# Performance work log

Hardware: AMD Instinct MI355X
Metric: run time of the kernel (lower is better)

The kernel has to match this reference:

```python
import jax, jax.numpy as jnp
import numpy as np

N_FEATURES = 256
SEQ_LEN = 128
N_HIDDEN = 30
N_LAYERS = 2
BATCH = 1024


def _lstm_layer(x, w_ih, w_hh, b_ih, b_hh):
    # x: [B, T, I]; w_ih: [4H, I]; w_hh: [4H, H]; biases: [4H]
    # PyTorch gate order: i, f, g, o
    B = x.shape[0]
    H = w_hh.shape[1]
    # precompute input contribution for all timesteps: [B, T, 4H]
    xg = jnp.einsum('bti,gi->btg', x, w_ih) + (b_ih + b_hh)
    xg = jnp.swapaxes(xg, 0, 1)  # [T, B, 4H]

    def step(carry, xg_t):
        h, c = carry
        gates = xg_t + h @ w_hh.T  # [B, 4H]
        i, f, g, o = jnp.split(gates, 4, axis=-1)
        i = jax.nn.sigmoid(i)
        f = jax.nn.sigmoid(f)
        g = jnp.tanh(g)
        o = jax.nn.sigmoid(o)
        c = f * c + i * g
        h = o * jnp.tanh(c)
        return (h, c), h

    h0 = jnp.zeros((B, H), dtype=x.dtype)
    c0 = jnp.zeros((B, H), dtype=x.dtype)
    _, hs = jax.lax.scan(step, (h0, c0), xg)
    return jnp.swapaxes(hs, 0, 1)  # [B, T, H]


def setup_inputs() -> dict:
    key = jax.random.key(0)
    ks = jax.random.split(key, 12)
    s_in = 1.0 / np.sqrt(N_HIDDEN)
    G = 4 * N_HIDDEN
    inp = {
        'x': jax.random.normal(ks[0], (BATCH, SEQ_LEN, N_FEATURES), dtype=jnp.float32),
        'w_ih0': jax.random.uniform(ks[1], (G, N_FEATURES), jnp.float32, -s_in, s_in),
        'w_hh0': jax.random.uniform(ks[2], (G, N_HIDDEN), jnp.float32, -s_in, s_in),
        'b_ih0': jax.random.uniform(ks[3], (G,), jnp.float32, -s_in, s_in),
        'b_hh0': jax.random.uniform(ks[4], (G,), jnp.float32, -s_in, s_in),
        'w_ih1': jax.random.uniform(ks[5], (G, N_HIDDEN), jnp.float32, -s_in, s_in),
        'w_hh1': jax.random.uniform(ks[6], (G, N_HIDDEN), jnp.float32, -s_in, s_in),
        'b_ih1': jax.random.uniform(ks[7], (G,), jnp.float32, -s_in, s_in),
        'b_hh1': jax.random.uniform(ks[8], (G,), jnp.float32, -s_in, s_in),
        'w_lin': jax.random.uniform(ks[9], (1, N_HIDDEN * SEQ_LEN), jnp.float32, -s_in, s_in),
        'b_lin': jax.random.uniform(ks[10], (1,), jnp.float32, -s_in, s_in),
    }
    return inp


def reference(x, w_ih0, w_hh0, b_ih0, b_hh0, w_ih1, w_hh1, b_ih1, b_hh1, w_lin, b_lin):
    h1 = _lstm_layer(x, w_ih0, w_hh0, b_ih0, b_hh0)   # [B, T, H]
    h2 = _lstm_layer(h1, w_ih1, w_hh1, b_ih1, b_hh1)  # [B, T, H]
    flat = h2.reshape(h2.shape[0], -1)                 # [B, T*H]
    return flat @ w_lin.T + b_lin                      # [B, 1]
```

## Files before the change

### kernel.cpp

```cpp
#include <hip/hip_runtime.h>

#define T_SEQ 128
#define NF 256
#define NH 30
#define NG 120
#define NBATCH 1024
#define M_ROWS (NBATCH * T_SEQ)

#define BIAS_OFF 0
#define BHI_OFF  1024
#define BLO_OFF  (BHI_OFF + 65536)
#define XG_OFF_B (BLO_OFF + 65536)

typedef __attribute__((ext_vector_type(8))) short short8;
typedef __attribute__((ext_vector_type(4))) float float4v;

__device__ __forceinline__ short bf16_of(float f) {
  union { float f; unsigned u; } v; v.f = f;
  unsigned r = v.u + 0x7fffu + ((v.u >> 16) & 1u);
  return (short)(r >> 16);
}
__device__ __forceinline__ float f_of_bf16(short s) {
  union { unsigned u; float f; } v; v.u = ((unsigned)(unsigned short)s) << 16;
  return v.f;
}

__device__ __forceinline__ float rl(float v, int j) {
  return __int_as_float(__builtin_amdgcn_readlane(__float_as_int(v), j));
}
__device__ __forceinline__ float fast_rcp(float x) { return __builtin_amdgcn_rcpf(x); }
__device__ __forceinline__ float act_mix(float x, float kIn, float kOut, float cOut) {
  float e = __expf(-kIn * x);
  float r = fast_rcp(1.0f + e);
  return fmaf(kOut, r, cOut);
}
__device__ __forceinline__ float tanh_fast(float x) {
  float e = __expf(-2.0f * x);
  float r = fast_rcp(1.0f + e);
  return fmaf(2.0f, r, -1.0f);
}

__global__ void prep_kernel(const float* __restrict__ w_ih0,
                            const float* __restrict__ b_ih0,
                            const float* __restrict__ b_hh0,
                            unsigned char* __restrict__ ws) {
  int gid = blockIdx.x * 256 + threadIdx.x;
  float* bias = (float*)(ws + BIAS_OFF);
  if (gid < 128) bias[gid] = (gid < NG) ? (b_ih0[gid] + b_hh0[gid]) : 0.0f;

  int lane = gid & 63;
  int ts = gid >> 6;
  int t = ts >> 3, s = ts & 7;
  int n = s * 16 + (lane & 15);
  int k0 = t * 32 + (lane >> 4) * 8;

  short8 hi, lo;
#pragma unroll
  for (int j = 0; j < 8; ++j) {
    float v = (n < NG) ? w_ih0[n * NF + k0 + j] : 0.0f;
    short h = bf16_of(v);
    hi[j] = h;
    lo[j] = bf16_of(v - f_of_bf16(h));
  }
  *(short8*)(ws + BHI_OFF + (size_t)gid * 16) = hi;
  *(short8*)(ws + BLO_OFF + (size_t)gid * 16) = lo;
}

__global__ __launch_bounds__(256, 3) void gemm_xg(const float* __restrict__ x,
                                                  const unsigned char* __restrict__ ws,
                                                  float* __restrict__ xg) {
  __shared__ short lds_B[2][8 * 2 * 64 * 8];
  const int tid = threadIdx.x;
  const int lane = tid & 63;
  const int wave = tid >> 6;
  const int r15 = lane & 15;
  const int quad = lane >> 4;
  const int rowbase = blockIdx.x * 128 + wave * 32;

  const short* __restrict__ Bhi = (const short*)(ws + BHI_OFF);
  const short* __restrict__ Blo = (const short*)(ws + BLO_OFF);
  const float* __restrict__ bias = (const float*)(ws + BIAS_OFF);

  float4v acc[2][8];
#pragma unroll
  for (int s = 0; s < 8; ++s) {
    float b = bias[s * 16 + r15];
    float4v bv = {b, b, b, b};
    acc[0][s] = bv;
    acc[1][s] = bv;
  }

  const float* xptr[2];
  xptr[0] = x + (size_t)(rowbase + r15) * NF + quad * 8;
  xptr[1] = x + (size_t)(rowbase + 16 + r15) * NF + quad * 8;

#pragma unroll
  for (int i = 0; i < 2; ++i) {
    int s = wave * 2 + i;
    const short* ghi = Bhi + ((size_t)(0 * 8 + s) * 64 + lane) * 8;
    const short* glo = Blo + ((size_t)(0 * 8 + s) * 64 + lane) * 8;
    short* lhi = &lds_B[0][(s * 2 + 0) * 64 * 8];
    short* llo = &lds_B[0][(s * 2 + 1) * 64 * 8];
    __builtin_amdgcn_global_load_lds((const __attribute__((address_space(1))) void*)ghi,
                                     (__attribute__((address_space(3))) void*)lhi, 16, 0, 0);
    __builtin_amdgcn_global_load_lds((const __attribute__((address_space(1))) void*)glo,
                                     (__attribute__((address_space(3))) void*)llo, 16, 0, 0);
  }

  short8 ahi[2], alo[2];
#pragma unroll
  for (int g = 0; g < 2; ++g) {
    float4 p0 = *(const float4*)(xptr[g] + 0);
    float4 p1 = *(const float4*)(xptr[g] + 4);
    float f[8] = {p0.x, p0.y, p0.z, p0.w, p1.x, p1.y, p1.z, p1.w};
#pragma unroll
    for (int j = 0; j < 8; ++j) {
      short h = bf16_of(f[j]);
      ahi[g][j] = h;
      alo[g][j] = bf16_of(f[j] - f_of_bf16(h));
    }
  }
  __syncthreads();

  for (int t = 0; t < 8; ++t) {
    const int buf = t & 1;
    float4 anx[2][2];
    if (t < 7) {
#pragma unroll
      for (int i = 0; i < 2; ++i) {
        int s = wave * 2 + i;
        const short* ghi = Bhi + ((size_t)((t + 1) * 8 + s) * 64 + lane) * 8;
        const short* glo = Blo + ((size_t)((t + 1) * 8 + s) * 64 + lane) * 8;
        short* lhi = &lds_B[buf ^ 1][(s * 2 + 0) * 64 * 8];
        short* llo = &lds_B[buf ^ 1][(s * 2 + 1) * 64 * 8];
        __builtin_amdgcn_global_load_lds((const __attribute__((address_space(1))) void*)ghi,
                                         (__attribute__((address_space(3))) void*)lhi, 16, 0, 0);
        __builtin_amdgcn_global_load_lds((const __attribute__((address_space(1))) void*)glo,
                                         (__attribute__((address_space(3))) void*)llo, 16, 0, 0);
      }
#pragma unroll
      for (int g = 0; g < 2; ++g) {
        anx[g][0] = *(const float4*)(xptr[g] + (t + 1) * 32);
        anx[g][1] = *(const float4*)(xptr[g] + (t + 1) * 32 + 4);
      }
    }

#pragma unroll
    for (int s = 0; s < 8; ++s) {
      const short8 bh = *(const short8*)&lds_B[buf][((s * 2 + 0) * 64 + lane) * 8];
      const short8 bl = *(const short8*)&lds_B[buf][((s * 2 + 1) * 64 + lane) * 8];
#pragma unroll
      for (int g = 0; g < 2; ++g) {
        acc[g][s] = __builtin_amdgcn_mfma_f32_16x16x32_bf16(ahi[g], bh, acc[g][s], 0, 0, 0);
        acc[g][s] = __builtin_amdgcn_mfma_f32_16x16x32_bf16(ahi[g], bl, acc[g][s], 0, 0, 0);
        acc[g][s] = __builtin_amdgcn_mfma_f32_16x16x32_bf16(alo[g], bh, acc[g][s], 0, 0, 0);
      }
    }

    if (t < 7) {
#pragma unroll
      for (int g = 0; g < 2; ++g) {
        float f[8] = {anx[g][0].x, anx[g][0].y, anx[g][0].z, anx[g][0].w,
                      anx[g][1].x, anx[g][1].y, anx[g][1].z, anx[g][1].w};
#pragma unroll
        for (int j = 0; j < 8; ++j) {
          short h = bf16_of(f[j]);
          ahi[g][j] = h;
          alo[g][j] = bf16_of(f[j] - f_of_bf16(h));
        }
      }
    }
    __syncthreads();
  }

#pragma unroll
  for (int g = 0; g < 2; ++g) {
    const int row0 = rowbase + g * 16 + quad * 4;
#pragma unroll
    for (int s = 0; s < 8; ++s) {
      const int col = s * 16 + r15;
      if (col < NG) {
#pragma unroll
        for (int i = 0; i < 4; ++i) {
          xg[(size_t)(row0 + i) * NG + col] = acc[g][s][i];
        }
      }
    }
  }
}

__global__ __launch_bounds__(64) void lstm_fused(const float* __restrict__ xg,
                                                 const float* __restrict__ w_hh0,
                                                 const float* __restrict__ w_ih1,
                                                 const float* __restrict__ w_hh1,
                                                 const float* __restrict__ b_ih1,
                                                 const float* __restrict__ b_hh1,
                                                 const float* __restrict__ w_lin,
                                                 const float* __restrict__ b_lin,
                                                 float* __restrict__ out) {
  const int b = blockIdx.x;
  const int lane = threadIdx.x;
  const bool hiHalf = lane >= 32;
  const int l = hiHalf ? (lane - 32) : lane;
  const int lc = (l < NH) ? l : (NH - 1);
  const int gA = hiHalf ? (60 + lc) : lc;
  const int gB = gA + NH;

  const float kInA = hiHalf ? 2.0f : 1.0f;
  const float kOutA = hiHalf ? 2.0f : 1.0f;
  const float cOutA = hiHalf ? -1.0f : 0.0f;

  float wA0[NH], wB0[NH], vA1[NH], vB1[NH], uA1[NH], uB1[NH];
#pragma unroll
  for (int j = 0; j < NH; ++j) {
    wA0[j] = w_hh0[gA * NH + j];
    wB0[j] = w_hh0[gB * NH + j];
    vA1[j] = w_ih1[gA * NH + j];
    vB1[j] = w_ih1[gB * NH + j];
    uA1[j] = w_hh1[gA * NH + j];
    uB1[j] = w_hh1[gB * NH + j];
  }
  const float bA1 = b_ih1[gA] + b_hh1[gA];
  const float bB1 = b_ih1[gB] + b_hh1[gB];

  float h0 = 0.0f, c0 = 0.0f, h1 = 0.0f, c1 = 0.0f, acc = 0.0f;
  const float* __restrict__ xgb = xg + (size_t)b * T_SEQ * NG;

  float xa[4], xb[4], wlr[4];
#pragma unroll
  for (int p = 0; p < 3; ++p) {
    xa[p] = xgb[p * NG + gA];
    xb[p] = xgb[p * NG + gB];
    wlr[p] = w_lin[p * NH + lc];
  }

#pragma unroll 4
  for (int t = 0; t < T_SEQ; ++t) {
    const int cur = t & 3;
    const int nxt = (t + 3) & 3;
    const int tp = (t + 3 < T_SEQ) ? (t + 3) : (T_SEQ - 1);
    float pxa = xgb[tp * NG + gA];
    float pxb = xgb[tp * NG + gB];
    float pwl = w_lin[tp * NH + lc];

    float sA = xa[cur], sB = xb[cur], sA2 = 0.0f, sB2 = 0.0f;
#pragma unroll
    for (int j = 0; j < NH; j += 2) {
      float hj = rl(h0, j);
      float hj1 = rl(h0, j + 1);
      sA = fmaf(hj, wA0[j], sA);
      sB = fmaf(hj, wB0[j], sB);
      sA2 = fmaf(hj1, wA0[j + 1], sA2);
      sB2 = fmaf(hj1, wB0[j + 1], sB2);
    }
    sA += sA2;
    sB += sB2;
    float aA = act_mix(sA, kInA, kOutA, cOutA);
    float aB = act_mix(sB, 1.0f, 1.0f, 0.0f);
    float gg = __shfl_down(aA, 32);
    float oo = __shfl_down(aB, 32);
    c0 = fmaf(aB, c0, aA * gg);
    h0 = oo * tanh_fast(c0);

    float sv = bA1, sv2 = 0.0f, svB = bB1, svB2 = 0.0f;
    float su = 0.0f, su2 = 0.0f, suB = 0.0f, suB2 = 0.0f;
#pragma unroll
    for (int j = 0; j < NH; j += 2) {
      float xj = rl(h0, j);
      float xj1 = rl(h0, j + 1);
      float hj = rl(h1, j);
      float hj1 = rl(h1, j + 1);
      sv = fmaf(xj, vA1[j], sv);
      svB = fmaf(xj, vB1[j], svB);
      sv2 = fmaf(xj1, vA1[j + 1], sv2);
      svB2 = fmaf(xj1, vB1[j + 1], svB2);
      su = fmaf(hj, uA1[j], su);
      suB = fmaf(hj, uB1[j], suB);
      su2 = fmaf(hj1, uA1[j + 1], su2);
      suB2 = fmaf(hj1, uB1[j + 1], suB2);
    }
    float s1A = (sv + sv2) + (su + su2);
    float s1B = (svB + svB2) + (suB + suB2);
    float a1A = act_mix(s1A, kInA, kOutA, cOutA);
    float a1B = act_mix(s1B, 1.0f, 1.0f, 0.0f);
    float gg1 = __shfl_down(a1A, 32);
    float oo1 = __shfl_down(a1B, 32);
    c1 = fmaf(a1B, c1, a1A * gg1);
    h1 = oo1 * tanh_fast(c1);

    acc = fmaf(h1, wlr[cur], acc);

    xa[nxt] = pxa;
    xb[nxt] = pxb;
    wlr[nxt] = pwl;
  }

  if (lane >= NH) acc = 0.0f;
#pragma unroll
  for (int off = 32; off > 0; off >>= 1) acc += __shfl_xor(acc, off);
  if (lane == 0) out[b] = acc + b_lin[0];
}

extern "C" void kernel_launch(void* const* d_in, const int* in_sizes, int n_in,
                              void* d_out, int out_size, void* d_ws, size_t ws_size,
                              hipStream_t stream) {
  (void)in_sizes; (void)n_in; (void)out_size; (void)ws_size;
  const float* x     = (const float*)d_in[0];
  const float* w_ih0 = (const float*)d_in[1];
  const float* w_hh0 = (const float*)d_in[2];
  const float* b_ih0 = (const float*)d_in[3];
  const float* b_hh0 = (const float*)d_in[4];
  const float* w_ih1 = (const float*)d_in[5];
  const float* w_hh1 = (const float*)d_in[6];
  const float* b_ih1 = (const float*)d_in[7];
  const float* b_hh1 = (const float*)d_in[8];
  const float* w_lin = (const float*)d_in[9];
  const float* b_lin = (const float*)d_in[10];
  unsigned char* ws = (unsigned char*)d_ws;
  float* out = (float*)d_out;
  float* xg = (float*)(ws + XG_OFF_B);

  prep_kernel<<<16, 256, 0, stream>>>(w_ih0, b_ih0, b_hh0, ws);
  gemm_xg<<<M_ROWS / 128, 256, 0, stream>>>(x, ws, xg);
  lstm_fused<<<NBATCH, 64, 0, stream>>>(xg, w_hh0, w_ih1, w_hh1,
                                        b_ih1, b_hh1, w_lin, b_lin, out);
}
```

Baseline: 294.1 us.

## Broadcast hidden state via LDS and use packed FP32 FMA in LSTM recurrence

Replaces per-element readlane broadcasts of the hidden state with a write to shared memory followed by vector reads. The recurrent dot products now use packed two-wide FMAs. Input-projection gate columns are interleaved in the prep kernel so each lane fetches its two gate preactivations with one 8-byte load, and activations use exp2 directly. The aim is to cut instruction count on the serial per-timestep chain, at the cost of LDS round-trip latency inside the dependency chain.

```diff
diff --git a/kernel.cpp b/kernel.cpp
--- a/kernel.cpp
+++ b/kernel.cpp
@@ -13,6 +13,7 @@
 #define XG_OFF_B (BLO_OFF + 65536)
 
 typedef __attribute__((ext_vector_type(8))) short short8;
+typedef __attribute__((ext_vector_type(2))) float float2v;
 typedef __attribute__((ext_vector_type(4))) float float4v;
 
 __device__ __forceinline__ short bf16_of(float f) {
@@ -25,19 +26,24 @@
   return v.f;
 }
 
-__device__ __forceinline__ float rl(float v, int j) {
-  return __int_as_float(__builtin_amdgcn_readlane(__float_as_int(v), j));
-}
 __device__ __forceinline__ float fast_rcp(float x) { return __builtin_amdgcn_rcpf(x); }
-__device__ __forceinline__ float act_mix(float x, float kIn, float kOut, float cOut) {
-  float e = __expf(-kIn * x);
-  float r = fast_rcp(1.0f + e);
-  return fmaf(kOut, r, cOut);
+
+#define L2E 1.4426950408889634f
+__device__ __forceinline__ float sigm_fast(float x) {
+  float e = __builtin_amdgcn_exp2f(-L2E * x);
+  return fast_rcp(1.0f + e);
+}
+__device__ __forceinline__ float act_a(float x, float kIn_l2, float kOut, float cOut) {
+  float e = __builtin_amdgcn_exp2f(-kIn_l2 * x);
+  return fmaf(kOut, fast_rcp(1.0f + e), cOut);
 }
 __device__ __forceinline__ float tanh_fast(float x) {
-  float e = __expf(-2.0f * x);
-  float r = fast_rcp(1.0f + e);
-  return fmaf(2.0f, r, -1.0f);
+  float e = __builtin_amdgcn_exp2f(-2.0f * L2E * x);
+  return fmaf(2.0f, fast_rcp(1.0f + e), -1.0f);
+}
+
+__device__ __forceinline__ float2v fma2(float2v a, float2v b, float2v c) {
+  return __builtin_elementwise_fma(a, b, c);
 }
 
 __global__ void prep_kernel(const float* __restrict__ w_ih0,
@@ -46,18 +52,22 @@
                             unsigned char* __restrict__ ws) {
   int gid = blockIdx.x * 256 + threadIdx.x;
   float* bias = (float*)(ws + BIAS_OFF);
-  if (gid < 128) bias[gid] = (gid < NG) ? (b_ih0[gid] + b_hh0[gid]) : 0.0f;
+  if (gid < 128) {
+    int og = (gid & 3) * NH + (gid >> 2);
+    bias[gid] = (gid < NG) ? (b_ih0[og] + b_hh0[og]) : 0.0f;
+  }
 
   int lane = gid & 63;
   int ts = gid >> 6;
   int t = ts >> 3, s = ts & 7;
   int n = s * 16 + (lane & 15);
+  int orig = (n & 3) * NH + (n >> 2);
   int k0 = t * 32 + (lane >> 4) * 8;
 
   short8 hi, lo;
 #pragma unroll
   for (int j = 0; j < 8; ++j) {
-    float v = (n < NG) ? w_ih0[n * NF + k0 + j] : 0.0f;
+    float v = (n < NG) ? w_ih0[orig * NF + k0 + j] : 0.0f;
     short h = bf16_of(v);
     hi[j] = h;
     lo[j] = bf16_of(v - f_of_bf16(h));
@@ -189,15 +199,17 @@
   }
 }
 
-__global__ __launch_bounds__(64) void lstm_fused(const float* __restrict__ xg,
-                                                 const float* __restrict__ w_hh0,
-                                                 const float* __restrict__ w_ih1,
-                                                 const float* __restrict__ w_hh1,
-                                                 const float* __restrict__ b_ih1,
-                                                 const float* __restrict__ b_hh1,
-                                                 const float* __restrict__ w_lin,
-                                                 const float* __restrict__ b_lin,
-                                                 float* __restrict__ out) {
+__global__ __launch_bounds__(64, 1) void lstm_fused(const float* __restrict__ xg,
+                                                    const float* __restrict__ w_hh0,
+                                                    const float* __restrict__ w_ih1,
+                                                    const float* __restrict__ w_hh1,
+                                                    const float* __restrict__ b_ih1,
+                                                    const float* __restrict__ b_hh1,
+                                                    const float* __restrict__ w_lin,
+                                                    const float* __restrict__ b_lin,
+                                                    float* __restrict__ out) {
+  __shared__ __align__(16) float hbuf0[32];
+  __shared__ __align__(16) float hbuf1[32];
   const int b = blockIdx.x;
   const int lane = threadIdx.x;
   const bool hiHalf = lane >= 32;
@@ -206,31 +218,39 @@
   const int gA = hiHalf ? (60 + lc) : lc;
   const int gB = gA + NH;
 
-  const float kInA = hiHalf ? 2.0f : 1.0f;
+  const float kInA = (hiHalf ? 2.0f : 1.0f) * L2E;
   const float kOutA = hiHalf ? 2.0f : 1.0f;
   const float cOutA = hiHalf ? -1.0f : 0.0f;
 
-  float wA0[NH], wB0[NH], vA1[NH], vB1[NH], uA1[NH], uB1[NH];
-#pragma unroll
-  for (int j = 0; j < NH; ++j) {
-    wA0[j] = w_hh0[gA * NH + j];
-    wB0[j] = w_hh0[gB * NH + j];
-    vA1[j] = w_ih1[gA * NH + j];
-    vB1[j] = w_ih1[gB * NH + j];
-    uA1[j] = w_hh1[gA * NH + j];
-    uB1[j] = w_hh1[gB * NH + j];
+  float2v W0A[15], W0B[15], V1A[15], V1B[15], U1A[15], U1B[15];
+#pragma unroll
+  for (int p = 0; p < 15; ++p) {
+    W0A[p] = *(const float2v*)&w_hh0[gA * NH + 2 * p];
+    W0B[p] = *(const float2v*)&w_hh0[gB * NH + 2 * p];
+    V1A[p] = *(const float2v*)&w_ih1[gA * NH + 2 * p];
+    V1B[p] = *(const float2v*)&w_ih1[gB * NH + 2 * p];
+    U1A[p] = *(const float2v*)&w_hh1[gA * NH + 2 * p];
+    U1B[p] = *(const float2v*)&w_hh1[gB * NH + 2 * p];
   }
   const float bA1 = b_ih1[gA] + b_hh1[gA];
   const float bB1 = b_ih1[gB] + b_hh1[gB];
 
-  float h0 = 0.0f, c0 = 0.0f, h1 = 0.0f, c1 = 0.0f, acc = 0.0f;
+  float4v h0q[8], h1q[8];
+#pragma unroll
+  for (int k = 0; k < 8; ++k) {
+    h0q[k] = float4v{0.f, 0.f, 0.f, 0.f};
+    h1q[k] = float4v{0.f, 0.f, 0.f, 0.f};
+  }
+
+  float c0 = 0.0f, c1 = 0.0f, acc = 0.0f;
   const float* __restrict__ xgb = xg + (size_t)b * T_SEQ * NG;
-
-  float xa[4], xb[4], wlr[4];
+  const int xoff = 4 * lc + (hiHalf ? 2 : 0);
+
+  float2v xab[4];
+  float wlr[4];
 #pragma unroll
   for (int p = 0; p < 3; ++p) {
-    xa[p] = xgb[p * NG + gA];
-    xb[p] = xgb[p * NG + gB];
+    xab[p] = *(const float2v*)&xgb[p * NG + xoff];
     wlr[p] = w_lin[p * NH + lc];
   }
 
@@ -239,59 +259,76 @@
     const int cur = t & 3;
     const int nxt = (t + 3) & 3;
     const int tp = (t + 3 < T_SEQ) ? (t + 3) : (T_SEQ - 1);
-    float pxa = xgb[tp * NG + gA];
-    float pxb = xgb[tp * NG + gB];
+    float2v pxg = *(const float2v*)&xgb[tp * NG + xoff];
     float pwl = w_lin[tp * NH + lc];
 
-    float sA = xa[cur], sB = xb[cur], sA2 = 0.0f, sB2 = 0.0f;
-#pragma unroll
-    for (int j = 0; j < NH; j += 2) {
-      float hj = rl(h0, j);
-      float hj1 = rl(h0, j + 1);
-      sA = fmaf(hj, wA0[j], sA);
-      sB = fmaf(hj, wB0[j], sB);
-      sA2 = fmaf(hj1, wA0[j + 1], sA2);
-      sB2 = fmaf(hj1, wB0[j + 1], sB2);
-    }
-    sA += sA2;
-    sB += sB2;
-    float aA = act_mix(sA, kInA, kOutA, cOutA);
-    float aB = act_mix(sB, 1.0f, 1.0f, 0.0f);
+    float2v a0A = {xab[cur].x, 0.f};
+    float2v a0B = {xab[cur].y, 0.f};
+#pragma unroll
+    for (int k = 0; k < 8; ++k) {
+      float2v hlo = __builtin_shufflevector(h0q[k], h0q[k], 0, 1);
+      a0A = fma2(hlo, W0A[2 * k], a0A);
+      a0B = fma2(hlo, W0B[2 * k], a0B);
+      if (k < 7) {
+        float2v hhi = __builtin_shufflevector(h0q[k], h0q[k], 2, 3);
+        a0A = fma2(hhi, W0A[2 * k + 1], a0A);
+        a0B = fma2(hhi, W0B[2 * k + 1], a0B);
+      }
+    }
+    float sA = a0A.x + a0A.y;
+    float sB = a0B.x + a0B.y;
+    float aA = act_a(sA, kInA, kOutA, cOutA);
+    float aB = sigm_fast(sB);
     float gg = __shfl_down(aA, 32);
     float oo = __shfl_down(aB, 32);
     c0 = fmaf(aB, c0, aA * gg);
-    h0 = oo * tanh_fast(c0);
-
-    float sv = bA1, sv2 = 0.0f, svB = bB1, svB2 = 0.0f;
-    float su = 0.0f, su2 = 0.0f, suB = 0.0f, suB2 = 0.0f;
-#pragma unroll
-    for (int j = 0; j < NH; j += 2) {
-      float xj = rl(h0, j);
-      float xj1 = rl(h0, j + 1);
-      float hj = rl(h1, j);
-      float hj1 = rl(h1, j + 1);
-      sv = fmaf(xj, vA1[j], sv);
-      svB = fmaf(xj, vB1[j], svB);
-      sv2 = fmaf(xj1, vA1[j + 1], sv2);
-      svB2 = fmaf(xj1, vB1[j + 1], svB2);
-      su = fmaf(hj, uA1[j], su);
-      suB = fmaf(hj, uB1[j], suB);
-      su2 = fmaf(hj1, uA1[j + 1], su2);
-      suB2 = fmaf(hj1, uB1[j + 1], suB2);
-    }
-    float s1A = (sv + sv2) + (su + su2);
-    float s1B = (svB + svB2) + (suB + suB2);
-    float a1A = act_mix(s1A, kInA, kOutA, cOutA);
-    float a1B = act_mix(s1B, 1.0f, 1.0f, 0.0f);
+    float h0 = oo * tanh_fast(c0);
+    if (lane < NH) hbuf0[lane] = h0;
+#pragma unroll
+    for (int k = 0; k < 8; ++k) h0q[k] = *(const float4v*)&hbuf0[4 * k];
+
+    float2v aUA = {bA1, 0.f};
+    float2v aUB = {bB1, 0.f};
+#pragma unroll
+    for (int k = 0; k < 8; ++k) {
+      float2v hlo = __builtin_shufflevector(h1q[k], h1q[k], 0, 1);
+      aUA = fma2(hlo, U1A[2 * k], aUA);
+      aUB = fma2(hlo, U1B[2 * k], aUB);
+      if (k < 7) {
+        float2v hhi = __builtin_shufflevector(h1q[k], h1q[k], 2, 3);
+        aUA = fma2(hhi, U1A[2 * k + 1], aUA);
+        aUB = fma2(hhi, U1B[2 * k + 1], aUB);
+      }
+    }
+
+    float2v aVA = {0.f, 0.f};
+    float2v aVB = {0.f, 0.f};
+#pragma unroll
+    for (int k = 0; k < 8; ++k) {
+      float2v hlo = __builtin_shufflevector(h0q[k], h0q[k], 0, 1);
+      aVA = fma2(hlo, V1A[2 * k], aVA);
+      aVB = fma2(hlo, V1B[2 * k], aVB);
+      if (k < 7) {
+        float2v hhi = __builtin_shufflevector(h0q[k], h0q[k], 2, 3);
+        aVA = fma2(hhi, V1A[2 * k + 1], aVA);
+        aVB = fma2(hhi, V1B[2 * k + 1], aVB);
+      }
+    }
+    float s1A = (aUA.x + aUA.y) + (aVA.x + aVA.y);
+    float s1B = (aUB.x + aUB.y) + (aVB.x + aVB.y);
+    float a1A = act_a(s1A, kInA, kOutA, cOutA);
+    float a1B = sigm_fast(s1B);
     float gg1 = __shfl_down(a1A, 32);
     float oo1 = __shfl_down(a1B, 32);
     c1 = fmaf(a1B, c1, a1A * gg1);
-    h1 = oo1 * tanh_fast(c1);
+    float h1 = oo1 * tanh_fast(c1);
+    if (lane < NH) hbuf1[lane] = h1;
+#pragma unroll
+    for (int k = 0; k < 8; ++k) h1q[k] = *(const float4v*)&hbuf1[4 * k];
 
     acc = fmaf(h1, wlr[cur], acc);
 
-    xa[nxt] = pxa;
-    xb[nxt] = pxb;
+    xab[nxt] = pxg;
     wlr[nxt] = pwl;
   }
 
```

Result: slower. 302.3 us (+2.8%).

## Interleave gate columns, packed bf16 split, and reorder LSTM recurrence

Applied to the files above, without the earlier changes.

Gate columns of w_ih0 and the bias are permuted so the xg row stores each unit's gate pair next to each other, letting the LSTM kernel fetch both gate inputs with one float2 load. The GEMM's fp32-to-bf16 hi/lo split now uses the packed v_cvt_pk_bf16_f32 instruction instead of scalar bit manipulation. In the recurrent kernel, the layer-1 hidden-hidden product is computed before layer 0's activations so it can overlap them, and h0 is broadcast once into a register array that both dot products reuse. Activations switch to exp2-based intrinsics. The cost is extra registers for the broadcast array, and the packed conversion's rounding may differ slightly from the old manual rounding.

```diff
diff --git a/kernel.cpp b/kernel.cpp
--- a/kernel.cpp
+++ b/kernel.cpp
@@ -29,15 +29,39 @@
   return __int_as_float(__builtin_amdgcn_readlane(__float_as_int(v), j));
 }
 __device__ __forceinline__ float fast_rcp(float x) { return __builtin_amdgcn_rcpf(x); }
-__device__ __forceinline__ float act_mix(float x, float kIn, float kOut, float cOut) {
-  float e = __expf(-kIn * x);
-  float r = fast_rcp(1.0f + e);
-  return fmaf(kOut, r, cOut);
+
+#define L2E 1.4426950408889634f
+__device__ __forceinline__ float sigm_fast(float x) {
+  float e = __builtin_amdgcn_exp2f(-L2E * x);
+  return fast_rcp(1.0f + e);
+}
+__device__ __forceinline__ float act_a(float x, float kIn_l2, float kOut, float cOut) {
+  float e = __builtin_amdgcn_exp2f(-kIn_l2 * x);
+  return fmaf(kOut, fast_rcp(1.0f + e), cOut);
 }
 __device__ __forceinline__ float tanh_fast(float x) {
-  float e = __expf(-2.0f * x);
-  float r = fast_rcp(1.0f + e);
-  return fmaf(2.0f, r, -1.0f);
+  float e = __builtin_amdgcn_exp2f(-2.0f * L2E * x);
+  return fmaf(2.0f, fast_rcp(1.0f + e), -1.0f);
+}
+
+__device__ __forceinline__ void cvt_split8(const float4 p0, const float4 p1,
+                                           short8& hi, short8& lo) {
+  union { short8 s; unsigned u[4]; } H, L;
+  float f[8] = {p0.x, p0.y, p0.z, p0.w, p1.x, p1.y, p1.z, p1.w};
+#pragma unroll
+  for (int p = 0; p < 4; ++p) {
+    float a = f[2 * p], c = f[2 * p + 1];
+    unsigned hp;
+    asm("v_cvt_pk_bf16_f32 %0, %1, %2" : "=v"(hp) : "v"(a), "v"(c));
+    float ra = a - __uint_as_float(hp << 16);
+    float rc = c - __uint_as_float(hp & 0xffff0000u);
+    unsigned lp;
+    asm("v_cvt_pk_bf16_f32 %0, %1, %2" : "=v"(lp) : "v"(ra), "v"(rc));
+    H.u[p] = hp;
+    L.u[p] = lp;
+  }
+  hi = H.s;
+  lo = L.s;
 }
 
 __global__ void prep_kernel(const float* __restrict__ w_ih0,
@@ -46,18 +70,22 @@
                             unsigned char* __restrict__ ws) {
   int gid = blockIdx.x * 256 + threadIdx.x;
   float* bias = (float*)(ws + BIAS_OFF);
-  if (gid < 128) bias[gid] = (gid < NG) ? (b_ih0[gid] + b_hh0[gid]) : 0.0f;
+  if (gid < 128) {
+    int og = (gid & 3) * NH + (gid >> 2);
+    bias[gid] = (gid < NG) ? (b_ih0[og] + b_hh0[og]) : 0.0f;
+  }
 
   int lane = gid & 63;
   int ts = gid >> 6;
   int t = ts >> 3, s = ts & 7;
   int n = s * 16 + (lane & 15);
+  int orig = (n & 3) * NH + (n >> 2);
   int k0 = t * 32 + (lane >> 4) * 8;
 
   short8 hi, lo;
 #pragma unroll
   for (int j = 0; j < 8; ++j) {
-    float v = (n < NG) ? w_ih0[n * NF + k0 + j] : 0.0f;
+    float v = (n < NG) ? w_ih0[orig * NF + k0 + j] : 0.0f;
     short h = bf16_of(v);
     hi[j] = h;
     lo[j] = bf16_of(v - f_of_bf16(h));
@@ -112,13 +140,7 @@
   for (int g = 0; g < 2; ++g) {
     float4 p0 = *(const float4*)(xptr[g] + 0);
     float4 p1 = *(const float4*)(xptr[g] + 4);
-    float f[8] = {p0.x, p0.y, p0.z, p0.w, p1.x, p1.y, p1.z, p1.w};
-#pragma unroll
-    for (int j = 0; j < 8; ++j) {
-      short h = bf16_of(f[j]);
-      ahi[g][j] = h;
-      alo[g][j] = bf16_of(f[j] - f_of_bf16(h));
-    }
+    cvt_split8(p0, p1, ahi[g], alo[g]);
   }
   __syncthreads();
 
@@ -160,14 +182,7 @@
     if (t < 7) {
 #pragma unroll
       for (int g = 0; g < 2; ++g) {
-        float f[8] = {anx[g][0].x, anx[g][0].y, anx[g][0].z, anx[g][0].w,
-                      anx[g][1].x, anx[g][1].y, anx[g][1].z, anx[g][1].w};
-#pragma unroll
-        for (int j = 0; j < 8; ++j) {
-          short h = bf16_of(f[j]);
-          ahi[g][j] = h;
-          alo[g][j] = bf16_of(f[j] - f_of_bf16(h));
-        }
+        cvt_split8(anx[g][0], anx[g][1], ahi[g], alo[g]);
       }
     }
     __syncthreads();
@@ -189,15 +204,15 @@
   }
 }
 
-__global__ __launch_bounds__(64) void lstm_fused(const float* __restrict__ xg,
-                                                 const float* __restrict__ w_hh0,
-                                                 const float* __restrict__ w_ih1,
-                                                 const float* __restrict__ w_hh1,
-                                                 const float* __restrict__ b_ih1,
-                                                 const float* __restrict__ b_hh1,
-                                                 const float* __restrict__ w_lin,
-                                                 const float* __restrict__ b_lin,
-                                                 float* __restrict__ out) {
+__global__ __launch_bounds__(64, 1) void lstm_fused(const float* __restrict__ xg,
+                                                    const float* __restrict__ w_hh0,
+                                                    const float* __restrict__ w_ih1,
+                                                    const float* __restrict__ w_hh1,
+                                                    const float* __restrict__ b_ih1,
+                                                    const float* __restrict__ b_hh1,
+                                                    const float* __restrict__ w_lin,
+                                                    const float* __restrict__ b_lin,
+                                                    float* __restrict__ out) {
   const int b = blockIdx.x;
   const int lane = threadIdx.x;
   const bool hiHalf = lane >= 32;
@@ -206,31 +221,36 @@
   const int gA = hiHalf ? (60 + lc) : lc;
   const int gB = gA + NH;
 
-  const float kInA = hiHalf ? 2.0f : 1.0f;
+  const float kInA = (hiHalf ? 2.0f : 1.0f) * L2E;
   const float kOutA = hiHalf ? 2.0f : 1.0f;
   const float cOutA = hiHalf ? -1.0f : 0.0f;
 
-  float wA0[NH], wB0[NH], vA1[NH], vB1[NH], uA1[NH], uB1[NH];
+  float W0A[NH], W0B[NH], V1A[NH], V1B[NH], U1A[NH], U1B[NH];
 #pragma unroll
   for (int j = 0; j < NH; ++j) {
-    wA0[j] = w_hh0[gA * NH + j];
-    wB0[j] = w_hh0[gB * NH + j];
-    vA1[j] = w_ih1[gA * NH + j];
-    vB1[j] = w_ih1[gB * NH + j];
-    uA1[j] = w_hh1[gA * NH + j];
-    uB1[j] = w_hh1[gB * NH + j];
+    W0A[j] = w_hh0[gA * NH + j];
+    W0B[j] = w_hh0[gB * NH + j];
+    V1A[j] = w_ih1[gA * NH + j];
+    V1B[j] = w_ih1[gB * NH + j];
+    U1A[j] = w_hh1[gA * NH + j];
+    U1B[j] = w_hh1[gB * NH + j];
   }
   const float bA1 = b_ih1[gA] + b_hh1[gA];
   const float bB1 = b_ih1[gB] + b_hh1[gB];
 
-  float h0 = 0.0f, c0 = 0.0f, h1 = 0.0f, c1 = 0.0f, acc = 0.0f;
+  float hs0[NH];
+#pragma unroll
+  for (int j = 0; j < NH; ++j) hs0[j] = 0.0f;
+  float h1 = 0.0f, c0 = 0.0f, c1 = 0.0f, acc = 0.0f;
+
   const float* __restrict__ xgb = xg + (size_t)b * T_SEQ * NG;
-
-  float xa[4], xb[4], wlr[4];
+  const int xoff = 4 * lc + (hiHalf ? 2 : 0);
+
+  float2 xab[4];
+  float wlr[4];
 #pragma unroll
   for (int p = 0; p < 3; ++p) {
-    xa[p] = xgb[p * NG + gA];
-    xb[p] = xgb[p * NG + gB];
+    xab[p] = *(const float2*)&xgb[p * NG + xoff];
     wlr[p] = w_lin[p * NH + lc];
   }
 
@@ -239,59 +259,57 @@
     const int cur = t & 3;
     const int nxt = (t + 3) & 3;
     const int tp = (t + 3 < T_SEQ) ? (t + 3) : (T_SEQ - 1);
-    float pxa = xgb[tp * NG + gA];
-    float pxb = xgb[tp * NG + gB];
+    float2 px = *(const float2*)&xgb[tp * NG + xoff];
     float pwl = w_lin[tp * NH + lc];
 
-    float sA = xa[cur], sB = xb[cur], sA2 = 0.0f, sB2 = 0.0f;
+    float sA = xab[cur].x, sB = xab[cur].y, sA2 = 0.0f, sB2 = 0.0f;
 #pragma unroll
     for (int j = 0; j < NH; j += 2) {
-      float hj = rl(h0, j);
-      float hj1 = rl(h0, j + 1);
-      sA = fmaf(hj, wA0[j], sA);
-      sB = fmaf(hj, wB0[j], sB);
-      sA2 = fmaf(hj1, wA0[j + 1], sA2);
-      sB2 = fmaf(hj1, wB0[j + 1], sB2);
-    }
-    sA += sA2;
-    sB += sB2;
-    float aA = act_mix(sA, kInA, kOutA, cOutA);
-    float aB = act_mix(sB, 1.0f, 1.0f, 0.0f);
+      sA  = fmaf(hs0[j],     W0A[j],     sA);
+      sB  = fmaf(hs0[j],     W0B[j],     sB);
+      sA2 = fmaf(hs0[j + 1], W0A[j + 1], sA2);
+      sB2 = fmaf(hs0[j + 1], W0B[j + 1], sB2);
+    }
+
+    float suA = bA1, suB = bB1, suA2 = 0.0f, suB2 = 0.0f;
+#pragma unroll
+    for (int j = 0; j < NH; j += 2) {
+      float hj = rl(h1, j);
+      float hj1 = rl(h1, j + 1);
+      suA  = fmaf(hj,  U1A[j],     suA);
+      suB  = fmaf(hj,  U1B[j],     suB);
+      suA2 = fmaf(hj1, U1A[j + 1], suA2);
+      suB2 = fmaf(hj1, U1B[j + 1], suB2);
+    }
+
+    float aA = act_a(sA + sA2, kInA, kOutA, cOutA);
+    float aB = sigm_fast(sB + sB2);
     float gg = __shfl_down(aA, 32);
     float oo = __shfl_down(aB, 32);
     c0 = fmaf(aB, c0, aA * gg);
-    h0 = oo * tanh_fast(c0);
-
-    float sv = bA1, sv2 = 0.0f, svB = bB1, svB2 = 0.0f;
-    float su = 0.0f, su2 = 0.0f, suB = 0.0f, suB2 = 0.0f;
+    float h0 = oo * tanh_fast(c0);
+
+#pragma unroll
+    for (int j = 0; j < NH; ++j) hs0[j] = rl(h0, j);
+
+    float svA = 0.0f, svB = 0.0f, svA2 = 0.0f, svB2 = 0.0f;
 #pragma unroll
     for (int j = 0; j < NH; j += 2) {
-      float xj = rl(h0, j);
-      float xj1 = rl(h0, j + 1);
-      float hj = rl(h1, j);
-      float hj1 = rl(h1, j + 1);
-      sv = fmaf(xj, vA1[j], sv);
-      svB = fmaf(xj, vB1[j], svB);
-      sv2 = fmaf(xj1, vA1[j + 1], sv2);
-      svB2 = fmaf(xj1, vB1[j + 1], svB2);
-      su = fmaf(hj, uA1[j], su);
-      suB = fmaf(hj, uB1[j], suB);
-      su2 = fmaf(hj1, uA1[j + 1], su2);
-      suB2 = fmaf(hj1, uB1[j + 1], suB2);
-    }
-    float s1A = (sv + sv2) + (su + su2);
-    float s1B = (svB + svB2) + (suB + suB2);
-    float a1A = act_mix(s1A, kInA, kOutA, cOutA);
-    float a1B = act_mix(s1B, 1.0f, 1.0f, 0.0f);
+      svA  = fmaf(hs0[j],     V1A[j],     svA);
+      svB  = fmaf(hs0[j],     V1B[j],     svB);
+      svA2 = fmaf(hs0[j + 1], V1A[j + 1], svA2);
+      svB2 = fmaf(hs0[j + 1], V1B[j + 1], svB2);
+    }
+
+    float a1A = act_a((suA + suA2) + (svA + svA2), kInA, kOutA, cOutA);
+    float a1B = sigm_fast((suB + suB2) + (svB + svB2));
     float gg1 = __shfl_down(a1A, 32);
     float oo1 = __shfl_down(a1B, 32);
     c1 = fmaf(a1B, c1, a1A * gg1);
     h1 = oo1 * tanh_fast(c1);
 
     acc = fmaf(h1, wlr[cur], acc);
-
-    xa[nxt] = pxa;
-    xb[nxt] = pxb;
+    xab[nxt] = px;
     wlr[nxt] = pwl;
   }
 
```

Measured after the change: 337.6 us. +14.8%, slower.
